# Optimization experiments

Measured on AMD Instinct MI355X. Metric: run time of the kernel, lower is better.

The kernel has to match this reference:

```python
import jax, jax.numpy as jnp
import numpy as np

NUM_HEADS = 16
ROPE_THETA = 10000.0


def _rope_cos_sin(seq_len, head_dim, dtype):
    # theta_i = theta^(-2i/d_k), i in [0, d_k/2)
    i = jnp.arange(head_dim // 2, dtype=jnp.float32)
    inv_freq = ROPE_THETA ** (-2.0 * i / head_dim)
    pos = jnp.arange(seq_len, dtype=jnp.float32)[:, None]
    ang = pos * inv_freq[None, :]                      # [S, d/2]
    return jnp.cos(ang).astype(dtype), jnp.sin(ang).astype(dtype)


def _apply_rope(t, cos, sin):
    # t: [B, H, S, d]; rotate consecutive pairs (complex multiply)
    B, H, S, d = t.shape
    tp = t.reshape(B, H, S, d // 2, 2)
    x0, x1 = tp[..., 0], tp[..., 1]
    r0 = x0 * cos - x1 * sin
    r1 = x0 * sin + x1 * cos
    return jnp.stack([r0, r1], axis=-1).reshape(B, H, S, d)


def setup_inputs() -> dict:
    key = jax.random.key(0)
    k1, k2, k3 = jax.random.split(key, 3)
    B, S, D = 4, 2048, 1024
    x = jax.random.normal(k1, (B, S, D), dtype=jnp.float32)
    padding_mask = jnp.ones((B, S), dtype=jnp.int32)
    # trunc-normal-ish init, std = sqrt(2/(in+out))
    std_qkv = np.sqrt(2.0 / (D + 3 * D))
    w_qkv = jax.random.normal(k2, (3 * D, D), dtype=jnp.float32) * std_qkv
    w_o = jax.random.normal(k3, (D, D), dtype=jnp.float32) * 0.02
    return {"x": x, "padding_mask": padding_mask, "w_qkv": w_qkv, "w_o": w_o}


def reference(x, padding_mask, w_qkv, w_o):
    B, S, D = x.shape
    H = NUM_HEADS
    hd = D // H
    scale = 1.0 / np.sqrt(hd)

    qkv = x @ w_qkv.T                                   # [B, S, 3D]
    q, k, v = jnp.split(qkv, 3, axis=-1)

    def to_heads(t):
        return t.reshape(B, S, H, hd).transpose(0, 2, 1, 3)  # [B, H, S, hd]

    q, k, v = to_heads(q), to_heads(k), to_heads(v)

    cos, sin = _rope_cos_sin(S, hd, x.dtype)            # [S, hd/2]
    q = _apply_rope(q, cos, sin)
    k = _apply_rope(k, cos, sin)

    scores = jnp.einsum("bhqd,bhkd->bhqk", q, k) * scale  # [B, H, S, S]

    causal = jnp.tril(jnp.ones((S, S), dtype=x.dtype))
    mask = causal[None, :, :] * padding_mask.astype(x.dtype)[:, None, :]  # [B, S, S]
    scores = jnp.where(mask[:, None, :, :] == 0, -jnp.inf, scores)

    weights = jax.nn.softmax(scores, axis=-1)
    out = jnp.einsum("bhqk,bhkd->bhqd", weights, v)     # [B, H, S, hd]
    out = out.transpose(0, 2, 1, 3).reshape(B, S, D)
    return out @ w_o.T
```

## Files before the change

### kernel.cpp

```cpp
#include <hip/hip_runtime.h>

typedef unsigned short u16;
typedef unsigned int u32;
typedef __bf16 bf16x8 __attribute__((ext_vector_type(8)));
typedef float f32x4 __attribute__((ext_vector_type(4)));
typedef float f32x16 __attribute__((ext_vector_type(16)));
typedef u32 u32x4 __attribute__((ext_vector_type(4)));

#define MFMA_BF16(a, b, c) __builtin_amdgcn_mfma_f32_16x16x32_bf16((a), (b), (c), 0, 0, 0)
#define MFMA32(a, b, c) __builtin_amdgcn_mfma_f32_32x32x16_bf16((a), (b), (c), 0, 0, 0)

#define QSCALE 0.18033688011112042f

#define BARRIER __builtin_amdgcn_s_barrier()
#define LGKM0                                                \
  do {                                                       \
    asm volatile("s_waitcnt lgkmcnt(0)" ::: "memory");       \
    __builtin_amdgcn_sched_barrier(0);                       \
  } while (0)
#define WAIT_VM(N) asm volatile("s_waitcnt vmcnt(" #N ")" ::: "memory")


__device__ __forceinline__ u16 f2bf(float f) {
  u32 u = __builtin_bit_cast(u32, f);
  u += 0x7fffu + ((u >> 16) & 1u);
  return (u16)(u >> 16);
}

__device__ __forceinline__ void async_copy16(const void* g, void* l) {
  __builtin_amdgcn_global_load_lds(
      (__attribute__((address_space(1))) void*)g,
      (__attribute__((address_space(3))) void*)l, 16, 0, 0);
}

__device__ __forceinline__ u32 cvt_pk_bf16(float lo, float hi) {
  u32 d;
  asm("v_cvt_pk_bf16_f32 %0, %1, %2" : "=v"(d) : "v"(lo), "v"(hi));
  return d;
}

__device__ __forceinline__ void swap32(u32& a, u32& b) {
  asm("v_permlane32_swap_b32 %0, %1" : "+v"(a), "+v"(b));
}


__global__ __launch_bounds__(256) void prep_kernel(
    const float* __restrict__ x_f, const float* __restrict__ wqkv_f,
    const float* __restrict__ wo_f, u16* __restrict__ xb,
    u16* __restrict__ wqkvb, u16* __restrict__ wob, float2* __restrict__ rope_t) {
  const int blk = blockIdx.x;
  if (blk < 12288) {
    const float* src;
    u16* dst;
    int base;
    float scale = 1.0f;
    if (blk < 8192)      { src = x_f;    dst = xb;    base = blk; }
    else if (blk < 11264){ src = wqkv_f; dst = wqkvb; base = blk - 8192;
                           if (base < 1024) scale = QSCALE; }
    else                 { src = wo_f;   dst = wob;   base = blk - 11264; }
    const int i = base * 1024 + threadIdx.x * 4;
    const float4 v = *(const float4*)(src + i);
    ushort4 o;
    o.x = f2bf(v.x * scale); o.y = f2bf(v.y * scale);
    o.z = f2bf(v.z * scale); o.w = f2bf(v.w * scale);
    *(ushort4*)(dst + i) = o;
  } else {
    const int idx = (blk - 12288) * 256 + threadIdx.x;
    const int s = idx >> 5, i = idx & 31;
    const float invf = __builtin_amdgcn_exp2f(-(float)i * 0.41524101186092027f);
    float rev = (float)s * invf * 0.15915494309189535f;
    rev -= floorf(rev);
    rope_t[idx] = make_float2(__builtin_amdgcn_cosf(rev), __builtin_amdgcn_sinf(rev));
  }
}


__device__ __forceinline__ void gemm256_bt(const u16* __restrict__ A,
                                           const u16* __restrict__ B,
                                           int row0, int col0, u16* lds,
                                           f32x4 acc[4][4]) {
  const int tid = threadIdx.x;
  const int wave = tid >> 6, lane = tid & 63;
  const int fr = lane & 15, quad = lane >> 4;
  const int wm = (wave >> 1) * 64;
  const int wn = (wave & 1) * 64;
  u16* bufA0 = lds;
  u16* bufB0 = lds + 16384;
  u16* bufA1 = lds + 24576;
  u16* bufB1 = lds + 40960;

  const int l8 = lane >> 3, l7 = lane & 7;
  const int csw = (l7 ^ l8) * 8;

  f32x4 zero = {0.f, 0.f, 0.f, 0.f};
#pragma unroll
  for (int mt = 0; mt < 4; ++mt)
#pragma unroll
    for (int nt = 0; nt < 4; ++nt) acc[mt][nt] = zero;

  auto stage = [&](int t) {
    u16* ba = (t & 1) ? bufA1 : bufA0;
    u16* bb = (t & 1) ? bufB1 : bufB0;
    const int k0 = t * 64;
#pragma unroll
    for (int c = 0; c < 4; ++c) {
      const int ch = c * 8 + wave;
      async_copy16(A + (size_t)(row0 + ch * 8 + l8) * 1024 + k0 + csw,
                   ba + ch * 512);
    }
#pragma unroll
    for (int c = 0; c < 2; ++c) {
      const int ch = c * 8 + wave;
      async_copy16(B + (size_t)(col0 + ch * 8 + l8) * 1024 + k0 + csw,
                   bb + ch * 512);
    }
  };

  const int f7 = fr & 7;
  const int sw0 = (quad ^ f7) * 8;
  const int sw1 = ((quad + 4) ^ f7) * 8;
  const int ar0 = (wm + fr) * 64, ar1 = (wm + 16 + fr) * 64;
  const int ar2 = (wm + 32 + fr) * 64, ar3 = (wm + 48 + fr) * 64;
  const int br0 = (wn + fr) * 64, br1 = (wn + 16 + fr) * 64;
  const int br2 = (wn + 32 + fr) * 64, br3 = (wn + 48 + fr) * 64;

  stage(0);
  stage(1);
  WAIT_VM(6);
  BARRIER;

  for (int t = 0; t < 16; ++t) {
    const u16* ba = (t & 1) ? bufA1 : bufA0;
    const u16* bb = (t & 1) ? bufB1 : bufB0;

    bf16x8 a0k0 = *(const bf16x8*)(ba + ar0 + sw0);
    bf16x8 a0k1 = *(const bf16x8*)(ba + ar0 + sw1);
    bf16x8 a1k0 = *(const bf16x8*)(ba + ar1 + sw0);
    bf16x8 a1k1 = *(const bf16x8*)(ba + ar1 + sw1);
    bf16x8 b0k0 = *(const bf16x8*)(bb + br0 + sw0);
    bf16x8 b0k1 = *(const bf16x8*)(bb + br0 + sw1);
    bf16x8 b1k0 = *(const bf16x8*)(bb + br1 + sw0);
    bf16x8 b1k1 = *(const bf16x8*)(bb + br1 + sw1);
    BARRIER;
    LGKM0;
    __builtin_amdgcn_s_setprio(1);
    acc[0][0] = MFMA_BF16(a0k0, b0k0, acc[0][0]);
    acc[0][1] = MFMA_BF16(a0k0, b1k0, acc[0][1]);
    acc[1][0] = MFMA_BF16(a1k0, b0k0, acc[1][0]);
    acc[1][1] = MFMA_BF16(a1k0, b1k0, acc[1][1]);
    acc[0][0] = MFMA_BF16(a0k1, b0k1, acc[0][0]);
    acc[0][1] = MFMA_BF16(a0k1, b1k1, acc[0][1]);
    acc[1][0] = MFMA_BF16(a1k1, b0k1, acc[1][0]);
    acc[1][1] = MFMA_BF16(a1k1, b1k1, acc[1][1]);
    __builtin_amdgcn_s_setprio(0);
    BARRIER;

    bf16x8 b2k0 = *(const bf16x8*)(bb + br2 + sw0);
    bf16x8 b2k1 = *(const bf16x8*)(bb + br2 + sw1);
    bf16x8 b3k0 = *(const bf16x8*)(bb + br3 + sw0);
    bf16x8 b3k1 = *(const bf16x8*)(bb + br3 + sw1);
    BARRIER;
    LGKM0;
    __builtin_amdgcn_s_setprio(1);
    acc[0][2] = MFMA_BF16(a0k0, b2k0, acc[0][2]);
    acc[0][3] = MFMA_BF16(a0k0, b3k0, acc[0][3]);
    acc[1][2] = MFMA_BF16(a1k0, b2k0, acc[1][2]);
    acc[1][3] = MFMA_BF16(a1k0, b3k0, acc[1][3]);
    acc[0][2] = MFMA_BF16(a0k1, b2k1, acc[0][2]);
    acc[0][3] = MFMA_BF16(a0k1, b3k1, acc[0][3]);
    acc[1][2] = MFMA_BF16(a1k1, b2k1, acc[1][2]);
    acc[1][3] = MFMA_BF16(a1k1, b3k1, acc[1][3]);
    __builtin_amdgcn_s_setprio(0);
    BARRIER;

    bf16x8 a2k0 = *(const bf16x8*)(ba + ar2 + sw0);
    bf16x8 a2k1 = *(const bf16x8*)(ba + ar2 + sw1);
    bf16x8 a3k0 = *(const bf16x8*)(ba + ar3 + sw0);
    bf16x8 a3k1 = *(const bf16x8*)(ba + ar3 + sw1);
    BARRIER;
    LGKM0;
    __builtin_amdgcn_s_setprio(1);
    acc[2][0] = MFMA_BF16(a2k0, b0k0, acc[2][0]);
    acc[2][1] = MFMA_BF16(a2k0, b1k0, acc[2][1]);
    acc[3][0] = MFMA_BF16(a3k0, b0k0, acc[3][0]);
    acc[3][1] = MFMA_BF16(a3k0, b1k0, acc[3][1]);
    acc[2][0] = MFMA_BF16(a2k1, b0k1, acc[2][0]);
    acc[2][1] = MFMA_BF16(a2k1, b1k1, acc[2][1]);
    acc[3][0] = MFMA_BF16(a3k1, b0k1, acc[3][0]);
    acc[3][1] = MFMA_BF16(a3k1, b1k1, acc[3][1]);
    acc[2][2] = MFMA_BF16(a2k0, b2k0, acc[2][2]);
    acc[2][3] = MFMA_BF16(a2k0, b3k0, acc[2][3]);
    acc[3][2] = MFMA_BF16(a3k0, b2k0, acc[3][2]);
    acc[3][3] = MFMA_BF16(a3k0, b3k0, acc[3][3]);
    acc[2][2] = MFMA_BF16(a2k1, b2k1, acc[2][2]);
    acc[2][3] = MFMA_BF16(a2k1, b3k1, acc[2][3]);
    acc[3][2] = MFMA_BF16(a3k1, b2k1, acc[3][2]);
    acc[3][3] = MFMA_BF16(a3k1, b3k1, acc[3][3]);
    __builtin_amdgcn_s_setprio(0);

    BARRIER;
    if (t + 2 < 16) {
      stage(t + 2);
      WAIT_VM(6);
    } else if (t + 2 == 16) {
      WAIT_VM(0);
    }
    BARRIER;
  }
}


__global__ __launch_bounds__(512, 2) void qkv_rope_kernel(
    const u16* __restrict__ x, const u16* __restrict__ w_qkv,
    const float2* __restrict__ rope_t,
    u16* __restrict__ q_ws, u16* __restrict__ k_ws, u16* __restrict__ vt_ws) {
  __shared__ u16 lds[49152];
  f32x4 acc[4][4];
  const int row0 = blockIdx.y * 256;
  const int col0 = blockIdx.x * 128;
  gemm256_bt(x, w_qkv, row0, col0, lds, acc);

  const int tid = threadIdx.x;
  const int wave = tid >> 6, lane = tid & 63;
  const int fr = lane & 15, quad = lane >> 4;
  const int wm = (wave >> 1) * 64, wn = (wave & 1) * 64;
  const int region = col0 >> 10;
  const int f0 = col0 & 1023;
  const int s0r = row0 & 2047;
  const int bb = row0 >> 11;
  const int h0 = f0 >> 6;

  if (region < 2) {
#pragma unroll
    for (int mt = 0; mt < 4; ++mt) {
#pragma unroll
      for (int nt = 0; nt < 4; ++nt) {
        const int n = wn + nt * 16 + fr;
        const int d = n & 63;
#pragma unroll
        for (int r = 0; r < 4; ++r) {
          const int m = wm + mt * 16 + quad * 4 + r;
          const float own = acc[mt][nt][r];
          const float part = __shfl_xor(own, 1);
          const int s = s0r + m;
          const float2 cssn = rope_t[s * 32 + (d >> 1)];
          const float val = (d & 1) ? (part * cssn.y + own * cssn.x)
                                    : (own * cssn.x - part * cssn.y);
          lds[m * 136 + n] = f2bf(val);
        }
      }
    }
    __syncthreads();
    u16* dst = (region == 0) ? q_ws : k_ws;
#pragma unroll
    for (int j = 0; j < 8; ++j) {
      const int idx2 = j * 512 + tid;
      const int m = idx2 >> 4;
      const int rem = idx2 & 15;
      const int hf = rem >> 3;
      const int c8 = (rem & 7) * 8;
      const uint4 v = *(const uint4*)(lds + m * 136 + hf * 64 + c8);
      *(uint4*)(dst + ((size_t)(bb * 16 + h0 + hf) * 2048 + s0r + m) * 64 + c8) = v;
    }
  } else {
#pragma unroll
    for (int mt = 0; mt < 4; ++mt)
#pragma unroll
      for (int nt = 0; nt < 4; ++nt) {
        const int n = wn + nt * 16 + fr;
#pragma unroll
        for (int r = 0; r < 4; ++r) {
          const int m = wm + mt * 16 + quad * 4 + r;
          lds[n * 264 + m] = f2bf(acc[mt][nt][r]);
        }
      }
    __syncthreads();
#pragma unroll
    for (int j = 0; j < 8; ++j) {
      const int idx2 = j * 512 + tid;
      const int n = idx2 >> 5;
      const int mc = (idx2 & 31) * 8;
      const int h = h0 + (n >> 6);
      const int d = n & 63;
      const uint4 v = *(const uint4*)(lds + n * 264 + mc);
      *(uint4*)(vt_ws + ((size_t)(bb * 16 + h) * 64 + d) * 2048 + s0r + mc) = v;
    }
  }
}


__global__ __launch_bounds__(256, 3) void flash_attn_kernel(
    const u16* __restrict__ Q, const u16* __restrict__ K, const u16* __restrict__ Vt,
    const int* __restrict__ pad, u16* __restrict__ O) {
  const int S = 2048;
  const int idx = blockIdx.x;
  const int bh = idx & 63;
  const int b = bh >> 4, h = bh & 15;
  const int j = (idx >> 6) & 3;
  const int sr = idx >> 8;
  const int qt_rev = (sr >> 1) * 8 + ((sr & 1) ? (7 - j) : j);
  const int q0 = (15 - qt_rev) * 128;
  const u16* Qh = Q + (size_t)bh * S * 64;
  const u16* Kh = K + (size_t)bh * S * 64;
  const u16* Vth = Vt + (size_t)bh * 64 * S;
  const int tid = threadIdx.x, wave = tid >> 6, lane = tid & 63;
  const int l31 = lane & 31, hi = lane >> 5, l7 = lane & 7;

  __shared__ u16 lds_k[2][64 * 64];
  __shared__ u16 lds_vt[2][64 * 64];
  __shared__ float lds_biasf[2][64];

  const int qb = q0 + wave * 32;

  bf16x8 qfrag[4];
#pragma unroll
  for (int c = 0; c < 4; ++c)
    qfrag[c] = *(const bf16x8*)(Qh + (size_t)(qb + l31) * 64 + c * 16 + hi * 8);

  bf16x8 ones;
#pragma unroll
  for (int jj = 0; jj < 8; ++jj) ones[jj] = (__bf16)1.0f;

  f32x16 o_acc0, o_acc1, lacc;
#pragma unroll
  for (int r = 0; r < 16; ++r) { o_acc0[r] = 0.f; o_acc1[r] = 0.f; lacc[r] = 0.f; }

  const float NEG = -__builtin_inff();
  int pv0 = 1, pv1 = 1;

  auto stage = [&](int k0, int bufi) {
#pragma unroll
    for (int it = 0; it < 2; ++it) {
      const int slot = it * 256 + tid;
      const int row = slot >> 3;
      const int g = slot & 7;
      const int gs = (g ^ (row & 7)) * 8;
      async_copy16(Kh + (size_t)(k0 + row) * 64 + gs, &lds_k[bufi][slot * 8]);
      async_copy16(Vth + (size_t)row * 2048 + k0 + gs, &lds_vt[bufi][slot * 8]);
    }
    if (tid < 64) lds_biasf[bufi][tid] = pad[b * S + k0 + tid] ? 0.f : NEG;
    const int pvn = pad[b * S + k0 + lane];
    if (bufi) pv1 = pvn; else pv0 = pvn;
  };

  const int kend = q0 + 64;
  stage(0, 0);
  __syncthreads();
  int cur = 0;

  for (int k0 = 0; k0 <= kend; k0 += 64) {
    if (k0 < kend) stage(k0 + 64, cur ^ 1);

    if (k0 <= qb + 31) {
      const u16* lk = lds_k[cur];
      const u16* lvt = lds_vt[cur];
      const float* lb = lds_biasf[cur];
      const int pvc = cur ? pv1 : pv0;
      const bool fast = (__ballot(pvc != 0) == ~0ull);
      const bool needMask = (k0 + 63 > qb);
      const int thrh = qb + l31 - k0 - 4 * hi;

      f32x16 sacc0, sacc1;
#pragma unroll
      for (int r = 0; r < 16; ++r) { sacc0[r] = 0.f; sacc1[r] = 0.f; }
#pragma unroll
      for (int c = 0; c < 4; ++c) {
        const int gsw = ((2 * c + hi) ^ l7) * 8;
        bf16x8 kf0 = *(const bf16x8*)(lk + l31 * 64 + gsw);
        bf16x8 kf1 = *(const bf16x8*)(lk + (l31 + 32) * 64 + gsw);
        sacc0 = MFMA32(kf0, qfrag[c], sacc0);
        sacc1 = MFMA32(kf1, qfrag[c], sacc1);
      }

      bf16x8 pa[2][2];
#pragma unroll
      for (int kt = 0; kt < 2; ++kt) {
        float pe[16];
        if (fast) {
#pragma unroll
          for (int r = 0; r < 16; ++r) {
            float s = (kt == 0) ? sacc0[r] : sacc1[r];
            if (needMask) {
              const int rm = (r & 3) + 8 * (r >> 2) + 32 * kt;
              s = (rm > thrh) ? NEG : s;
            }
            pe[r] = __builtin_amdgcn_exp2f(s);
          }
        } else {
          f32x4 bv[4];
#pragma unroll
          for (int g = 0; g < 4; ++g)
            bv[g] = *(const f32x4*)(lb + g * 8 + 4 * hi + 32 * kt);
#pragma unroll
          for (int r = 0; r < 16; ++r) {
            float s = ((kt == 0) ? sacc0[r] : sacc1[r]) + bv[r >> 2][r & 3];
            if (needMask) {
              const int rm = (r & 3) + 8 * (r >> 2) + 32 * kt;
              s = (rm > thrh) ? NEG : s;
            }
            pe[r] = __builtin_amdgcn_exp2f(s);
          }
        }
        u32 a0 = cvt_pk_bf16(pe[0], pe[1]), a1 = cvt_pk_bf16(pe[2], pe[3]);
        u32 b0 = cvt_pk_bf16(pe[4], pe[5]), b1 = cvt_pk_bf16(pe[6], pe[7]);
        swap32(a0, b0);
        swap32(a1, b1);
        u32x4 w0 = {a0, a1, b0, b1};
        pa[kt][0] = __builtin_bit_cast(bf16x8, w0);
        u32 c0 = cvt_pk_bf16(pe[8], pe[9]), c1 = cvt_pk_bf16(pe[10], pe[11]);
        u32 d0 = cvt_pk_bf16(pe[12], pe[13]), d1 = cvt_pk_bf16(pe[14], pe[15]);
        swap32(c0, d0);
        swap32(c1, d1);
        u32x4 w1 = {c0, c1, d0, d1};
        pa[kt][1] = __builtin_bit_cast(bf16x8, w1);
      }

      __builtin_amdgcn_s_setprio(1);
#pragma unroll
      for (int kt = 0; kt < 2; ++kt)
#pragma unroll
        for (int ks = 0; ks < 2; ++ks) {
          const int kq = kt * 2 + ks;
          lacc = MFMA32(pa[kt][ks], ones, lacc);
          const int gsw = ((2 * kq + hi) ^ l7) * 8;
          bf16x8 vf0 = *(const bf16x8*)(lvt + l31 * 64 + gsw);
          bf16x8 vf1 = *(const bf16x8*)(lvt + (l31 + 32) * 64 + gsw);
          o_acc0 = MFMA32(pa[kt][ks], vf0, o_acc0);
          o_acc1 = MFMA32(pa[kt][ks], vf1, o_acc1);
        }
      __builtin_amdgcn_s_setprio(0);
    }

    __syncthreads();
    cur ^= 1;
  }

#pragma unroll
  for (int r = 0; r < 16; ++r) {
    const int q = qb + (r & 3) + 8 * (r >> 2) + 4 * hi;
    const float l = lacc[r];
    const float rl = (l > 0.f) ? (1.0f / l) : 0.f;
    O[(size_t)(b * S + q) * 1024 + h * 64 + l31] = f2bf(o_acc0[r] * rl);
    O[(size_t)(b * S + q) * 1024 + h * 64 + 32 + l31] = f2bf(o_acc1[r] * rl);
  }
}


__global__ __launch_bounds__(512, 2) void oproj_kernel(
    const u16* __restrict__ A, const u16* __restrict__ w_o, float* __restrict__ out) {
  __shared__ u16 lds[49152];
  f32x4 acc[4][4];
  const int row0 = blockIdx.y * 256;
  const int col0 = blockIdx.x * 128;
  gemm256_bt(A, w_o, row0, col0, lds, acc);
  const int tid = threadIdx.x;
  const int wave = tid >> 6, lane = tid & 63;
  const int fr = lane & 15, quad = lane >> 4;
  const int wm = (wave >> 1) * 64, wn = (wave & 1) * 64;
#pragma unroll
  for (int mt = 0; mt < 4; ++mt)
#pragma unroll
    for (int nt = 0; nt < 4; ++nt) {
      const int ncol = col0 + wn + nt * 16 + fr;
#pragma unroll
      for (int r = 0; r < 4; ++r) {
        const int mrow = row0 + wm + mt * 16 + quad * 4 + r;
        out[(size_t)mrow * 1024 + ncol] = acc[mt][nt][r];
      }
    }
}


extern "C" void kernel_launch(void* const* d_in, const int* in_sizes, int n_in,
                              void* d_out, int out_size, void* d_ws, size_t ws_size,
                              hipStream_t stream) {
  const float* x_f = (const float*)d_in[0];
  const int* pad = (const int*)d_in[1];
  const float* wqkv_f = (const float*)d_in[2];
  const float* wo_f = (const float*)d_in[3];
  float* out = (float*)d_out;

  const int NX = 4 * 2048 * 1024;
  const int NWQKV = 3072 * 1024;
  const int NWO = 1024 * 1024;
  const size_t HSZ = (size_t)4 * 16 * 2048 * 64;

  u16* xb = (u16*)d_ws;
  u16* wqkvb = xb + NX;
  u16* wob = wqkvb + NWQKV;
  u16* q_ws = wob + NWO;
  u16* k_ws = q_ws + HSZ;
  u16* vt_ws = k_ws + HSZ;
  u16* attn_ws = vt_ws + HSZ;
  float2* rope_t = (float2*)(attn_ws + HSZ);

  prep_kernel<<<dim3(12544), dim3(256), 0, stream>>>(x_f, wqkv_f, wo_f, xb, wqkvb,
                                                     wob, rope_t);
  qkv_rope_kernel<<<dim3(24, 32), dim3(512), 0, stream>>>(xb, wqkvb, rope_t, q_ws,
                                                          k_ws, vt_ws);
  flash_attn_kernel<<<dim3(1024), dim3(256), 0, stream>>>(q_ws, k_ws, vt_ws, pad,
                                                          attn_ws);
  oproj_kernel<<<dim3(8, 32), dim3(512), 0, stream>>>(attn_ws, wob, out);
}
```

Measured before the change: 251.9 us.

## Enlarge QKV GEMM tile to 256x256 with two-pass epilogue

Replaces the 256x128 QKV projection tile with a 256x256 tile, giving each wave a 128x64 sub-tile with 32 accumulators and halving the grid to 12x32 blocks. The goal is more arithmetic per byte loaded from global memory and LDS, which improves data reuse in the GEMM. The epilogue now runs in two passes over 128-column halves so the existing LDS staging layout can be reused. In exchange the block uses 128KB of LDS and more accumulator registers, and with only 384 blocks occupancy drops and the wave on the 256 CUs becomes uneven.

```diff
diff --git a/kernel.cpp b/kernel.cpp
--- a/kernel.cpp
+++ b/kernel.cpp
@@ -75,6 +75,265 @@
 }
 
 
+__device__ __forceinline__ void gemm256sq(const u16* __restrict__ A,
+                                          const u16* __restrict__ B,
+                                          int row0, int col0, u16* lds,
+                                          f32x4 acc[8][4]) {
+  const int tid = threadIdx.x;
+  const int wave = tid >> 6, lane = tid & 63;
+  const int fr = lane & 15, quad = lane >> 4;
+  const int wr = wave >> 2, wc = wave & 3;
+  const int wm = wr * 128, wn = wc * 64;
+
+  f32x4 zero = {0.f, 0.f, 0.f, 0.f};
+#pragma unroll
+  for (int mt = 0; mt < 8; ++mt)
+#pragma unroll
+    for (int nt = 0; nt < 4; ++nt) acc[mt][nt] = zero;
+
+  auto stage = [&](int t) {
+    u16* ba = lds + ((t & 1) ? 32768 : 0);
+    u16* bb = lds + ((t & 1) ? 49152 : 16384);
+    const int k0 = t * 64;
+#pragma unroll
+    for (int it = 0; it < 4; ++it) {
+      const int slot = it * 512 + tid;
+      const int row = slot >> 3, g = slot & 7;
+      const int gs = (g ^ (row & 7)) * 8;
+      async_copy16(A + (size_t)(row0 + row) * 1024 + k0 + gs, ba + slot * 8);
+    }
+#pragma unroll
+    for (int it = 0; it < 4; ++it) {
+      const int slot = it * 512 + tid;
+      const int row = slot >> 3, g = slot & 7;
+      const int gs = (g ^ (row & 7)) * 8;
+      async_copy16(B + (size_t)(col0 + row) * 1024 + k0 + gs, bb + slot * 8);
+    }
+  };
+
+  const int swr = fr & 7;
+  const int sw0 = (quad ^ swr) * 8;
+  const int sw1 = ((quad + 4) ^ swr) * 8;
+
+  stage(0);
+  stage(1);
+  WAIT_VM(8);
+  BARRIER;
+
+  for (int t = 0; t < 16; ++t) {
+    const u16* ba = lds + ((t & 1) ? 32768 : 0);
+    const u16* bb = lds + ((t & 1) ? 49152 : 16384);
+
+    bf16x8 a0k0 = *(const bf16x8*)(ba + (wm + fr) * 64 + sw0);
+    bf16x8 a0k1 = *(const bf16x8*)(ba + (wm + fr) * 64 + sw1);
+    bf16x8 a1k0 = *(const bf16x8*)(ba + (wm + 16 + fr) * 64 + sw0);
+    bf16x8 a1k1 = *(const bf16x8*)(ba + (wm + 16 + fr) * 64 + sw1);
+    bf16x8 a2k0 = *(const bf16x8*)(ba + (wm + 32 + fr) * 64 + sw0);
+    bf16x8 a2k1 = *(const bf16x8*)(ba + (wm + 32 + fr) * 64 + sw1);
+    bf16x8 a3k0 = *(const bf16x8*)(ba + (wm + 48 + fr) * 64 + sw0);
+    bf16x8 a3k1 = *(const bf16x8*)(ba + (wm + 48 + fr) * 64 + sw1);
+    bf16x8 b0k0 = *(const bf16x8*)(bb + (wn + fr) * 64 + sw0);
+    bf16x8 b0k1 = *(const bf16x8*)(bb + (wn + fr) * 64 + sw1);
+    bf16x8 b1k0 = *(const bf16x8*)(bb + (wn + 16 + fr) * 64 + sw0);
+    bf16x8 b1k1 = *(const bf16x8*)(bb + (wn + 16 + fr) * 64 + sw1);
+    BARRIER;
+    LGKM0;
+    __builtin_amdgcn_s_setprio(1);
+    acc[0][0] = MFMA_BF16(a0k0, b0k0, acc[0][0]);
+    acc[0][1] = MFMA_BF16(a0k0, b1k0, acc[0][1]);
+    acc[1][0] = MFMA_BF16(a1k0, b0k0, acc[1][0]);
+    acc[1][1] = MFMA_BF16(a1k0, b1k0, acc[1][1]);
+    acc[2][0] = MFMA_BF16(a2k0, b0k0, acc[2][0]);
+    acc[2][1] = MFMA_BF16(a2k0, b1k0, acc[2][1]);
+    acc[3][0] = MFMA_BF16(a3k0, b0k0, acc[3][0]);
+    acc[3][1] = MFMA_BF16(a3k0, b1k0, acc[3][1]);
+    acc[0][0] = MFMA_BF16(a0k1, b0k1, acc[0][0]);
+    acc[0][1] = MFMA_BF16(a0k1, b1k1, acc[0][1]);
+    acc[1][0] = MFMA_BF16(a1k1, b0k1, acc[1][0]);
+    acc[1][1] = MFMA_BF16(a1k1, b1k1, acc[1][1]);
+    acc[2][0] = MFMA_BF16(a2k1, b0k1, acc[2][0]);
+    acc[2][1] = MFMA_BF16(a2k1, b1k1, acc[2][1]);
+    acc[3][0] = MFMA_BF16(a3k1, b0k1, acc[3][0]);
+    acc[3][1] = MFMA_BF16(a3k1, b1k1, acc[3][1]);
+    __builtin_amdgcn_s_setprio(0);
+    BARRIER;
+
+    bf16x8 b2k0 = *(const bf16x8*)(bb + (wn + 32 + fr) * 64 + sw0);
+    bf16x8 b2k1 = *(const bf16x8*)(bb + (wn + 32 + fr) * 64 + sw1);
+    bf16x8 b3k0 = *(const bf16x8*)(bb + (wn + 48 + fr) * 64 + sw0);
+    bf16x8 b3k1 = *(const bf16x8*)(bb + (wn + 48 + fr) * 64 + sw1);
+    BARRIER;
+    LGKM0;
+    __builtin_amdgcn_s_setprio(1);
+    acc[0][2] = MFMA_BF16(a0k0, b2k0, acc[0][2]);
+    acc[0][3] = MFMA_BF16(a0k0, b3k0, acc[0][3]);
+    acc[1][2] = MFMA_BF16(a1k0, b2k0, acc[1][2]);
+    acc[1][3] = MFMA_BF16(a1k0, b3k0, acc[1][3]);
+    acc[2][2] = MFMA_BF16(a2k0, b2k0, acc[2][2]);
+    acc[2][3] = MFMA_BF16(a2k0, b3k0, acc[2][3]);
+    acc[3][2] = MFMA_BF16(a3k0, b2k0, acc[3][2]);
+    acc[3][3] = MFMA_BF16(a3k0, b3k0, acc[3][3]);
+    acc[0][2] = MFMA_BF16(a0k1, b2k1, acc[0][2]);
+    acc[0][3] = MFMA_BF16(a0k1, b3k1, acc[0][3]);
+    acc[1][2] = MFMA_BF16(a1k1, b2k1, acc[1][2]);
+    acc[1][3] = MFMA_BF16(a1k1, b3k1, acc[1][3]);
+    acc[2][2] = MFMA_BF16(a2k1, b2k1, acc[2][2]);
+    acc[2][3] = MFMA_BF16(a2k1, b3k1, acc[2][3]);
+    acc[3][2] = MFMA_BF16(a3k1, b2k1, acc[3][2]);
+    acc[3][3] = MFMA_BF16(a3k1, b3k1, acc[3][3]);
+    __builtin_amdgcn_s_setprio(0);
+    BARRIER;
+
+    bf16x8 a4k0 = *(const bf16x8*)(ba + (wm + 64 + fr) * 64 + sw0);
+    bf16x8 a4k1 = *(const bf16x8*)(ba + (wm + 64 + fr) * 64 + sw1);
+    bf16x8 a5k0 = *(const bf16x8*)(ba + (wm + 80 + fr) * 64 + sw0);
+    bf16x8 a5k1 = *(const bf16x8*)(ba + (wm + 80 + fr) * 64 + sw1);
+    bf16x8 a6k0 = *(const bf16x8*)(ba + (wm + 96 + fr) * 64 + sw0);
+    bf16x8 a6k1 = *(const bf16x8*)(ba + (wm + 96 + fr) * 64 + sw1);
+    bf16x8 a7k0 = *(const bf16x8*)(ba + (wm + 112 + fr) * 64 + sw0);
+    bf16x8 a7k1 = *(const bf16x8*)(ba + (wm + 112 + fr) * 64 + sw1);
+    BARRIER;
+    LGKM0;
+    __builtin_amdgcn_s_setprio(1);
+    acc[4][0] = MFMA_BF16(a4k0, b0k0, acc[4][0]);
+    acc[4][1] = MFMA_BF16(a4k0, b1k0, acc[4][1]);
+    acc[5][0] = MFMA_BF16(a5k0, b0k0, acc[5][0]);
+    acc[5][1] = MFMA_BF16(a5k0, b1k0, acc[5][1]);
+    acc[6][0] = MFMA_BF16(a6k0, b0k0, acc[6][0]);
+    acc[6][1] = MFMA_BF16(a6k0, b1k0, acc[6][1]);
+    acc[7][0] = MFMA_BF16(a7k0, b0k0, acc[7][0]);
+    acc[7][1] = MFMA_BF16(a7k0, b1k0, acc[7][1]);
+    acc[4][0] = MFMA_BF16(a4k1, b0k1, acc[4][0]);
+    acc[4][1] = MFMA_BF16(a4k1, b1k1, acc[4][1]);
+    acc[5][0] = MFMA_BF16(a5k1, b0k1, acc[5][0]);
+    acc[5][1] = MFMA_BF16(a5k1, b1k1, acc[5][1]);
+    acc[6][0] = MFMA_BF16(a6k1, b0k1, acc[6][0]);
+    acc[6][1] = MFMA_BF16(a6k1, b1k1, acc[6][1]);
+    acc[7][0] = MFMA_BF16(a7k1, b0k1, acc[7][0]);
+    acc[7][1] = MFMA_BF16(a7k1, b1k1, acc[7][1]);
+    __builtin_amdgcn_s_setprio(0);
+    BARRIER;
+
+    __builtin_amdgcn_s_setprio(1);
+    acc[4][2] = MFMA_BF16(a4k0, b2k0, acc[4][2]);
+    acc[4][3] = MFMA_BF16(a4k0, b3k0, acc[4][3]);
+    acc[5][2] = MFMA_BF16(a5k0, b2k0, acc[5][2]);
+    acc[5][3] = MFMA_BF16(a5k0, b3k0, acc[5][3]);
+    acc[6][2] = MFMA_BF16(a6k0, b2k0, acc[6][2]);
+    acc[6][3] = MFMA_BF16(a6k0, b3k0, acc[6][3]);
+    acc[7][2] = MFMA_BF16(a7k0, b2k0, acc[7][2]);
+    acc[7][3] = MFMA_BF16(a7k0, b3k0, acc[7][3]);
+    acc[4][2] = MFMA_BF16(a4k1, b2k1, acc[4][2]);
+    acc[4][3] = MFMA_BF16(a4k1, b3k1, acc[4][3]);
+    acc[5][2] = MFMA_BF16(a5k1, b2k1, acc[5][2]);
+    acc[5][3] = MFMA_BF16(a5k1, b3k1, acc[5][3]);
+    acc[6][2] = MFMA_BF16(a6k1, b2k1, acc[6][2]);
+    acc[6][3] = MFMA_BF16(a6k1, b3k1, acc[6][3]);
+    acc[7][2] = MFMA_BF16(a7k1, b2k1, acc[7][2]);
+    acc[7][3] = MFMA_BF16(a7k1, b3k1, acc[7][3]);
+    __builtin_amdgcn_s_setprio(0);
+
+    BARRIER;
+    if (t + 2 < 16) {
+      stage(t + 2);
+      WAIT_VM(8);
+    } else {
+      WAIT_VM(0);
+    }
+    BARRIER;
+  }
+}
+
+
+__global__ __launch_bounds__(512, 2) void qkv_rope_kernel(
+    const u16* __restrict__ x, const u16* __restrict__ w_qkv,
+    const float2* __restrict__ rope_t,
+    u16* __restrict__ q_ws, u16* __restrict__ k_ws, u16* __restrict__ vt_ws) {
+  __shared__ u16 lds[65536];
+  f32x4 acc[8][4];
+  const int row0 = blockIdx.y * 256;
+  const int col0 = blockIdx.x * 256;
+  gemm256sq(x, w_qkv, row0, col0, lds, acc);
+
+  const int tid = threadIdx.x;
+  const int wave = tid >> 6, lane = tid & 63;
+  const int fr = lane & 15, quad = lane >> 4;
+  const int wr = wave >> 2, wc = wave & 3;
+  const int wm = wr * 128;
+  const int region = col0 >> 10;
+  const int f0 = col0 & 1023;
+  const int s0r = row0 & 2047;
+  const int bb = row0 >> 11;
+  const int h0 = f0 >> 6;
+
+#pragma unroll
+  for (int hp = 0; hp < 2; ++hp) {
+    __syncthreads();
+    if ((wc >> 1) == hp) {
+      const int n1b = (wc & 1) * 64;
+      if (region < 2) {
+#pragma unroll
+        for (int mt = 0; mt < 8; ++mt)
+#pragma unroll
+          for (int nt = 0; nt < 4; ++nt) {
+            const int n1 = n1b + nt * 16 + fr;
+            const int d = n1 & 63;
+#pragma unroll
+            for (int r = 0; r < 4; ++r) {
+              const int m = wm + mt * 16 + quad * 4 + r;
+              const float own = acc[mt][nt][r];
+              const float part = __shfl_xor(own, 1);
+              const float2 cssn = rope_t[(s0r + m) * 32 + (d >> 1)];
+              const float val = (d & 1) ? (part * cssn.y + own * cssn.x)
+                                        : (own * cssn.x - part * cssn.y);
+              lds[m * 136 + n1] = f2bf(val);
+            }
+          }
+      } else {
+#pragma unroll
+        for (int mt = 0; mt < 8; ++mt)
+#pragma unroll
+          for (int nt = 0; nt < 4; ++nt) {
+            const int n1 = n1b + nt * 16 + fr;
+#pragma unroll
+            for (int r = 0; r < 4; ++r) {
+              const int m = wm + mt * 16 + quad * 4 + r;
+              lds[n1 * 264 + m] = f2bf(acc[mt][nt][r]);
+            }
+          }
+      }
+    }
+    __syncthreads();
+    if (region < 2) {
+      u16* dst = (region == 0) ? q_ws : k_ws;
+#pragma unroll
+      for (int j = 0; j < 8; ++j) {
+        const int idx2 = j * 512 + tid;
+        const int m = idx2 >> 4;
+        const int rem = idx2 & 15;
+        const int hf = rem >> 3;
+        const int c8 = (rem & 7) * 8;
+        const uint4 v = *(const uint4*)(lds + m * 136 + hf * 64 + c8);
+        *(uint4*)(dst + ((size_t)(bb * 16 + h0 + hp * 2 + hf) * 2048 + s0r + m) * 64 +
+                  c8) = v;
+      }
+    } else {
+#pragma unroll
+      for (int j = 0; j < 8; ++j) {
+        const int idx2 = j * 512 + tid;
+        const int n1 = idx2 >> 5;
+        const int mc = (idx2 & 31) * 8;
+        const int ng = hp * 128 + n1;
+        const int h = h0 + (ng >> 6);
+        const int d = ng & 63;
+        const uint4 v = *(const uint4*)(lds + n1 * 264 + mc);
+        *(uint4*)(vt_ws + ((size_t)(bb * 16 + h) * 64 + d) * 2048 + s0r + mc) = v;
+      }
+    }
+  }
+}
+
+
 __device__ __forceinline__ void gemm256_bt(const u16* __restrict__ A,
                                            const u16* __restrict__ B,
                                            int row0, int col0, u16* lds,
@@ -206,85 +465,6 @@
       WAIT_VM(0);
     }
     BARRIER;
-  }
-}
-
-
-__global__ __launch_bounds__(512, 2) void qkv_rope_kernel(
-    const u16* __restrict__ x, const u16* __restrict__ w_qkv,
-    const float2* __restrict__ rope_t,
-    u16* __restrict__ q_ws, u16* __restrict__ k_ws, u16* __restrict__ vt_ws) {
-  __shared__ u16 lds[49152];
-  f32x4 acc[4][4];
-  const int row0 = blockIdx.y * 256;
-  const int col0 = blockIdx.x * 128;
-  gemm256_bt(x, w_qkv, row0, col0, lds, acc);
-
-  const int tid = threadIdx.x;
-  const int wave = tid >> 6, lane = tid & 63;
-  const int fr = lane & 15, quad = lane >> 4;
-  const int wm = (wave >> 1) * 64, wn = (wave & 1) * 64;
-  const int region = col0 >> 10;
-  const int f0 = col0 & 1023;
-  const int s0r = row0 & 2047;
-  const int bb = row0 >> 11;
-  const int h0 = f0 >> 6;
-
-  if (region < 2) {
-#pragma unroll
-    for (int mt = 0; mt < 4; ++mt) {
-#pragma unroll
-      for (int nt = 0; nt < 4; ++nt) {
-        const int n = wn + nt * 16 + fr;
-        const int d = n & 63;
-#pragma unroll
-        for (int r = 0; r < 4; ++r) {
-          const int m = wm + mt * 16 + quad * 4 + r;
-          const float own = acc[mt][nt][r];
-          const float part = __shfl_xor(own, 1);
-          const int s = s0r + m;
-          const float2 cssn = rope_t[s * 32 + (d >> 1)];
-          const float val = (d & 1) ? (part * cssn.y + own * cssn.x)
-                                    : (own * cssn.x - part * cssn.y);
-          lds[m * 136 + n] = f2bf(val);
-        }
-      }
-    }
-    __syncthreads();
-    u16* dst = (region == 0) ? q_ws : k_ws;
-#pragma unroll
-    for (int j = 0; j < 8; ++j) {
-      const int idx2 = j * 512 + tid;
-      const int m = idx2 >> 4;
-      const int rem = idx2 & 15;
-      const int hf = rem >> 3;
-      const int c8 = (rem & 7) * 8;
-      const uint4 v = *(const uint4*)(lds + m * 136 + hf * 64 + c8);
-      *(uint4*)(dst + ((size_t)(bb * 16 + h0 + hf) * 2048 + s0r + m) * 64 + c8) = v;
-    }
-  } else {
-#pragma unroll
-    for (int mt = 0; mt < 4; ++mt)
-#pragma unroll
-      for (int nt = 0; nt < 4; ++nt) {
-        const int n = wn + nt * 16 + fr;
-#pragma unroll
-        for (int r = 0; r < 4; ++r) {
-          const int m = wm + mt * 16 + quad * 4 + r;
-          lds[n * 264 + m] = f2bf(acc[mt][nt][r]);
-        }
-      }
-    __syncthreads();
-#pragma unroll
-    for (int j = 0; j < 8; ++j) {
-      const int idx2 = j * 512 + tid;
-      const int n = idx2 >> 5;
-      const int mc = (idx2 & 31) * 8;
-      const int h = h0 + (n >> 6);
-      const int d = n & 63;
-      const uint4 v = *(const uint4*)(lds + n * 264 + mc);
-      *(uint4*)(vt_ws + ((size_t)(bb * 16 + h) * 64 + d) * 2048 + s0r + mc) = v;
-    }
   }
 }
 
@@ -496,7 +676,7 @@
 
   prep_kernel<<<dim3(12544), dim3(256), 0, stream>>>(x_f, wqkv_f, wo_f, xb, wqkvb,
                                                      wob, rope_t);
-  qkv_rope_kernel<<<dim3(24, 32), dim3(512), 0, stream>>>(xb, wqkvb, rope_t, q_ws,
+  qkv_rope_kernel<<<dim3(12, 32), dim3(512), 0, stream>>>(xb, wqkvb, rope_t, q_ws,
                                                           k_ws, vt_ws);
   flash_attn_kernel<<<dim3(1024), dim3(256), 0, stream>>>(q_ws, k_ws, vt_ws, pad,
                                                           attn_ws);
```

New measurement: 264.9 us. 1.05x slower.

## Widen QKV GEMM tile to 256x256 with half-K staged pipeline

Applied to the files above, without the earlier changes.

Replaces the 256x128 QKV projection tile with a 256x256 tile in which each wave computes 128x64. The K dimension is split into 32-wide halves that are double-buffered and interleaved with MFMA phases, and the grid is halved to 12x32 blocks. The larger tile raises arithmetic intensity and reduces global re-reads of x and weights. In exchange, per-block LDS grows to 128KB, which limits occupancy, accumulator registers double, and the RoPE/transpose epilogue runs in two serialized passes.

```diff
diff --git a/kernel.cpp b/kernel.cpp
--- a/kernel.cpp
+++ b/kernel.cpp
@@ -75,6 +75,214 @@
 }
 
 
+__device__ __forceinline__ void gemm256x8(const u16* __restrict__ A,
+                                          const u16* __restrict__ B,
+                                          int row0, int col0, u16* lds,
+                                          f32x4 acc[8][4]) {
+  const int tid = threadIdx.x;
+  const int wave = tid >> 6, lane = tid & 63;
+  const int fr = lane & 15, quad = lane >> 4;
+  const int wr = wave >> 2, wc = wave & 3;
+  const int wm = wr * 128, wn = wc * 64;
+
+  f32x4 zero = {0.f, 0.f, 0.f, 0.f};
+#pragma unroll
+  for (int mt = 0; mt < 8; ++mt)
+#pragma unroll
+    for (int nt = 0; nt < 4; ++nt) acc[mt][nt] = zero;
+
+  auto stageH = [&](const u16* src, int baserow, int kcol, u16* dst) {
+#pragma unroll
+    for (int it = 0; it < 2; ++it) {
+      const int slot = it * 512 + tid;
+      const int row = slot >> 2, g = slot & 3;
+      const int glog = g ^ ((row >> 1) & 3);
+      async_copy16(src + (size_t)(baserow + row) * 1024 + kcol + glog * 8,
+                   dst + slot * 8);
+    }
+  };
+
+  const int rbase = fr * 32 + (quad ^ ((fr >> 1) & 3)) * 8;
+
+  u16* const d0 = lds;
+  u16* const d1 = lds + 32768;
+
+  stageH(A, row0, 0, d0);
+  stageH(B, col0, 0, d0 + 8192);
+  stageH(A, row0, 32, d0 + 16384);
+  stageH(B, col0, 32, d0 + 24576);
+  stageH(A, row0, 64, d1);
+  stageH(B, col0, 64, d1 + 8192);
+  WAIT_VM(4);
+  BARRIER;
+
+  for (int t = 0; t < 16; ++t) {
+    u16* const cb = (t & 1) ? d1 : d0;
+    u16* const ob = (t & 1) ? d0 : d1;
+    const int k0 = t * 64;
+
+    bf16x8 a[8], b[4];
+
+#pragma unroll
+    for (int m = 0; m < 4; ++m)
+      a[m] = *(const bf16x8*)(cb + (wm + m * 16) * 32 + rbase);
+#pragma unroll
+    for (int n = 0; n < 4; ++n)
+      b[n] = *(const bf16x8*)(cb + 8192 + (wn + n * 16) * 32 + rbase);
+    if (t + 1 < 16) stageH(A, row0, k0 + 96, ob + 16384);
+    BARRIER;
+    LGKM0;
+    __builtin_amdgcn_s_setprio(1);
+#pragma unroll
+    for (int m = 0; m < 4; ++m)
+#pragma unroll
+      for (int n = 0; n < 4; ++n)
+        acc[m][n] = MFMA_BF16(a[m], b[n], acc[m][n]);
+    __builtin_amdgcn_s_setprio(0);
+    BARRIER;
+
+#pragma unroll
+    for (int m = 0; m < 4; ++m)
+      a[4 + m] = *(const bf16x8*)(cb + (wm + 64 + m * 16) * 32 + rbase);
+    if (t + 1 < 16) stageH(B, col0, k0 + 96, ob + 24576);
+    BARRIER;
+    LGKM0;
+    __builtin_amdgcn_s_setprio(1);
+#pragma unroll
+    for (int m = 0; m < 4; ++m)
+#pragma unroll
+      for (int n = 0; n < 4; ++n)
+        acc[4 + m][n] = MFMA_BF16(a[4 + m], b[n], acc[4 + m][n]);
+    __builtin_amdgcn_s_setprio(0);
+    if (t < 15) { WAIT_VM(4); } else { WAIT_VM(0); }
+    BARRIER;
+
+#pragma unroll
+    for (int m = 0; m < 4; ++m)
+      a[m] = *(const bf16x8*)(cb + 16384 + (wm + m * 16) * 32 + rbase);
+#pragma unroll
+    for (int n = 0; n < 4; ++n)
+      b[n] = *(const bf16x8*)(cb + 24576 + (wn + n * 16) * 32 + rbase);
+    if (t + 2 < 16) stageH(A, row0, k0 + 128, cb);
+    BARRIER;
+    LGKM0;
+    __builtin_amdgcn_s_setprio(1);
+#pragma unroll
+    for (int m = 0; m < 4; ++m)
+#pragma unroll
+      for (int n = 0; n < 4; ++n)
+        acc[m][n] = MFMA_BF16(a[m], b[n], acc[m][n]);
+    __builtin_amdgcn_s_setprio(0);
+    BARRIER;
+
+#pragma unroll
+    for (int m = 0; m < 4; ++m)
+      a[4 + m] = *(const bf16x8*)(cb + 16384 + (wm + 64 + m * 16) * 32 + rbase);
+    if (t + 2 < 16) stageH(B, col0, k0 + 128, cb + 8192);
+    BARRIER;
+    LGKM0;
+    __builtin_amdgcn_s_setprio(1);
+#pragma unroll
+    for (int m = 0; m < 4; ++m)
+#pragma unroll
+      for (int n = 0; n < 4; ++n)
+        acc[4 + m][n] = MFMA_BF16(a[4 + m], b[n], acc[4 + m][n]);
+    __builtin_amdgcn_s_setprio(0);
+    if (t < 14) { WAIT_VM(4); } else { WAIT_VM(0); }
+    BARRIER;
+  }
+}
+
+
+__global__ __launch_bounds__(512, 2) void qkv_rope_kernel(
+    const u16* __restrict__ x, const u16* __restrict__ w_qkv,
+    const float2* __restrict__ rope_t,
+    u16* __restrict__ q_ws, u16* __restrict__ k_ws, u16* __restrict__ vt_ws) {
+  __shared__ u16 lds[65536];
+  f32x4 acc[8][4];
+  const int row0 = blockIdx.y * 256;
+  const int col0 = blockIdx.x * 256;
+  gemm256x8(x, w_qkv, row0, col0, lds, acc);
+
+  const int tid = threadIdx.x;
+  const int wave = tid >> 6, lane = tid & 63;
+  const int fr = lane & 15, quad = lane >> 4;
+  const int wr = wave >> 2, wc = wave & 3;
+  const int wm = wr * 128;
+  const int region = col0 >> 10;
+  const int f0 = col0 & 1023;
+  const int s0r = row0 & 2047;
+  const int bb = row0 >> 11;
+  const int h0 = f0 >> 6;
+
+#pragma unroll
+  for (int hp = 0; hp < 2; ++hp) {
+    __syncthreads();
+    if ((wc >> 1) == hp) {
+      const int n1b = (wc & 1) * 64;
+      if (region < 2) {
+#pragma unroll
+        for (int mt = 0; mt < 8; ++mt)
+#pragma unroll
+          for (int nt = 0; nt < 4; ++nt) {
+            const int n1 = n1b + nt * 16 + fr;
+            const int d = n1 & 63;
+#pragma unroll
+            for (int r = 0; r < 4; ++r) {
+              const int m = wm + mt * 16 + quad * 4 + r;
+              const float own = acc[mt][nt][r];
+              const float part = __shfl_xor(own, 1);
+              const float2 cssn = rope_t[(s0r + m) * 32 + (d >> 1)];
+              const float val = (d & 1) ? (part * cssn.y + own * cssn.x)
+                                        : (own * cssn.x - part * cssn.y);
+              lds[m * 136 + n1] = f2bf(val);
+            }
+          }
+      } else {
+#pragma unroll
+        for (int mt = 0; mt < 8; ++mt)
+#pragma unroll
+          for (int nt = 0; nt < 4; ++nt) {
+            const int n1 = n1b + nt * 16 + fr;
+#pragma unroll
+            for (int r = 0; r < 4; ++r) {
+              const int m = wm + mt * 16 + quad * 4 + r;
+              lds[n1 * 264 + m] = f2bf(acc[mt][nt][r]);
+            }
+          }
+      }
+    }
+    __syncthreads();
+    if (region < 2) {
+      u16* dst = (region == 0) ? q_ws : k_ws;
+#pragma unroll
+      for (int j = 0; j < 8; ++j) {
+        const int idx2 = j * 512 + tid;
+        const int m = idx2 >> 4;
+        const int rem = idx2 & 15;
+        const int hf = rem >> 3;
+        const int c8 = (rem & 7) * 8;
+        const uint4 v = *(const uint4*)(lds + m * 136 + hf * 64 + c8);
+        *(uint4*)(dst + ((size_t)(bb * 16 + h0 + hp * 2 + hf) * 2048 + s0r + m) * 64 +
+                  c8) = v;
+      }
+    } else {
+#pragma unroll
+      for (int j = 0; j < 8; ++j) {
+        const int idx2 = j * 512 + tid;
+        const int n1 = idx2 >> 5;
+        const int mc = (idx2 & 31) * 8;
+        const int ng = hp * 128 + n1;
+        const int h = h0 + (ng >> 6);
+        const int d = ng & 63;
+        const uint4 v = *(const uint4*)(lds + n1 * 264 + mc);
+        *(uint4*)(vt_ws + ((size_t)(bb * 16 + h) * 64 + d) * 2048 + s0r + mc) = v;
+      }
+    }
+  }
+}
+
+
 __device__ __forceinline__ void gemm256_bt(const u16* __restrict__ A,
                                            const u16* __restrict__ B,
                                            int row0, int col0, u16* lds,
@@ -206,85 +414,6 @@
       WAIT_VM(0);
     }
     BARRIER;
-  }
-}
-
-
-__global__ __launch_bounds__(512, 2) void qkv_rope_kernel(
-    const u16* __restrict__ x, const u16* __restrict__ w_qkv,
-    const float2* __restrict__ rope_t,
-    u16* __restrict__ q_ws, u16* __restrict__ k_ws, u16* __restrict__ vt_ws) {
-  __shared__ u16 lds[49152];
-  f32x4 acc[4][4];
-  const int row0 = blockIdx.y * 256;
-  const int col0 = blockIdx.x * 128;
-  gemm256_bt(x, w_qkv, row0, col0, lds, acc);
-
-  const int tid = threadIdx.x;
-  const int wave = tid >> 6, lane = tid & 63;
-  const int fr = lane & 15, quad = lane >> 4;
-  const int wm = (wave >> 1) * 64, wn = (wave & 1) * 64;
-  const int region = col0 >> 10;
-  const int f0 = col0 & 1023;
-  const int s0r = row0 & 2047;
-  const int bb = row0 >> 11;
-  const int h0 = f0 >> 6;
-
-  if (region < 2) {
-#pragma unroll
-    for (int mt = 0; mt < 4; ++mt) {
-#pragma unroll
-      for (int nt = 0; nt < 4; ++nt) {
-        const int n = wn + nt * 16 + fr;
-        const int d = n & 63;
-#pragma unroll
-        for (int r = 0; r < 4; ++r) {
-          const int m = wm + mt * 16 + quad * 4 + r;
-          const float own = acc[mt][nt][r];
-          const float part = __shfl_xor(own, 1);
-          const int s = s0r + m;
-          const float2 cssn = rope_t[s * 32 + (d >> 1)];
-          const float val = (d & 1) ? (part * cssn.y + own * cssn.x)
-                                    : (own * cssn.x - part * cssn.y);
-          lds[m * 136 + n] = f2bf(val);
-        }
-      }
-    }
-    __syncthreads();
-    u16* dst = (region == 0) ? q_ws : k_ws;
-#pragma unroll
-    for (int j = 0; j < 8; ++j) {
-      const int idx2 = j * 512 + tid;
-      const int m = idx2 >> 4;
-      const int rem = idx2 & 15;
-      const int hf = rem >> 3;
-      const int c8 = (rem & 7) * 8;
-      const uint4 v = *(const uint4*)(lds + m * 136 + hf * 64 + c8);
-      *(uint4*)(dst + ((size_t)(bb * 16 + h0 + hf) * 2048 + s0r + m) * 64 + c8) = v;
-    }
-  } else {
-#pragma unroll
-    for (int mt = 0; mt < 4; ++mt)
-#pragma unroll
-      for (int nt = 0; nt < 4; ++nt) {
-        const int n = wn + nt * 16 + fr;
-#pragma unroll
-        for (int r = 0; r < 4; ++r) {
-          const int m = wm + mt * 16 + quad * 4 + r;
-          lds[n * 264 + m] = f2bf(acc[mt][nt][r]);
-        }
-      }
-    __syncthreads();
-#pragma unroll
-    for (int j = 0; j < 8; ++j) {
-      const int idx2 = j * 512 + tid;
-      const int n = idx2 >> 5;
-      const int mc = (idx2 & 31) * 8;
-      const int h = h0 + (n >> 6);
-      const int d = n & 63;
-      const uint4 v = *(const uint4*)(lds + n * 264 + mc);
-      *(uint4*)(vt_ws + ((size_t)(bb * 16 + h) * 64 + d) * 2048 + s0r + mc) = v;
-    }
   }
 }
 
@@ -496,7 +625,7 @@
 
   prep_kernel<<<dim3(12544), dim3(256), 0, stream>>>(x_f, wqkv_f, wo_f, xb, wqkvb,
                                                      wob, rope_t);
-  qkv_rope_kernel<<<dim3(24, 32), dim3(512), 0, stream>>>(xb, wqkvb, rope_t, q_ws,
+  qkv_rope_kernel<<<dim3(12, 32), dim3(512), 0, stream>>>(xb, wqkvb, rope_t, q_ws,
                                                           k_ws, vt_ws);
   flash_attn_kernel<<<dim3(1024), dim3(256), 0, stream>>>(q_ws, k_ws, vt_ws, pad,
                                                           attn_ws);
```

New measurement: 262.0 us. 1.04x slower.
